# Optimization experiments

Measured on AMD Instinct MI355X. Metric: run time of the kernel, lower is better.

## Reference

```python
import jax, jax.numpy as jnp
import numpy as np

B, D, H, W, K = 32, 32, 256, 256, 512
N_TAGS = 30


def setup_inputs() -> dict:
    key = jax.random.key(0)
    k1, k2, k3 = jax.random.split(key, 3)
    ebd_batch = jax.random.normal(k1, (B, D, H, W), dtype=jnp.float32)
    # integer pixel coords (row, col) already in-range -> mask in original is all-true
    kpts = jax.random.randint(k2, (B, K, 2), 0, H).astype(jnp.int64)
    tags = jax.random.randint(k3, (B, K), 0, N_TAGS).astype(jnp.int64)
    return {"ebd_batch": ebd_batch, "kpts": kpts, "tags": tags}


def _per_image(ebd, kp, tg):
    # ebd: [D,H,W], kp: [K,2] int, tg: [K] int
    pred = ebd[:, kp[:, 0], kp[:, 1]]            # [D,K] gathered embeddings
    d = pred.shape[0]
    true_sim = (tg[:, None] == tg[None, :]).astype(pred.dtype)   # [K,K]
    # expo[k,l] = mean_d (pred[d,k]-pred[d,l])^2, via gram expansion (no DxKxK tensor)
    sq = jnp.mean(pred * pred, axis=0)           # [K]
    gram = jnp.einsum('dk,dl->kl', pred, pred) / d
    expo = sq[:, None] + sq[None, :] - 2.0 * gram
    pred_sim = 2.0 / (1.0 + jnp.exp(expo))
    return jnp.mean((true_sim - pred_sim) ** 2)


def reference(ebd_batch, kpts, tags):
    losses = jax.vmap(_per_image)(ebd_batch, kpts, tags)  # [B]
    return jnp.mean(losses)
```

## Files before the change

kernel.cpp:

```cpp
#include <hip/hip_runtime.h>

#define BB 32
#define DD 32
#define HH 256
#define WW 256
#define KK 512

typedef __attribute__((ext_vector_type(8))) short bf16x8;
typedef __attribute__((ext_vector_type(4))) float f32x4;

#define LO_OFF  (1u << 20)
#define SSQ_OFF (2u << 20)

__global__ __launch_bounds__(256) void tagloss_gather(
    const float* __restrict__ ebd, const int* __restrict__ kpts,
    char* __restrict__ ws, float* __restrict__ out) {
  int gid = blockIdx.x * 256 + threadIdx.x;
  if (gid == 0) out[0] = 0.f;
  int col = gid >> 5;
  int d   = gid & 31;
  int b   = col >> 9;

  int y = kpts[col * 2 + 0];
  int x = kpts[col * 2 + 1];
  float v = ebd[((size_t)(b * DD + d)) * (HH * WW) + (size_t)y * WW + x];

  unsigned u  = __float_as_uint(v);
  unsigned rn = u + 0x7FFFu + ((u >> 16) & 1u);
  float hif = __uint_as_float(rn & 0xFFFF0000u);
  float lof = v - hif;
  unsigned ul = __float_as_uint(lof);
  unsigned rl = ul + 0x7FFFu + ((ul >> 16) & 1u);

  ((ushort*)ws)[col * DD + d]            = (ushort)(rn >> 16);
  ((ushort*)(ws + LO_OFF))[col * DD + d] = (ushort)(rl >> 16);

  float s = v * v;
#pragma unroll
  for (int m = 16; m > 0; m >>= 1) s += __shfl_xor(s, m);
  if (d == 0) ((float*)(ws + SSQ_OFF))[col] = s;
}

__global__ __launch_bounds__(256, 2) void tagloss_pairs(
    const char* __restrict__ ws, const int* __restrict__ tags,
    float* __restrict__ out) {
  __shared__ __align__(16) char P[65536];
  __shared__ float ssqL[KK];
  __shared__ int   tagL[KK];
  __shared__ float red[4];

  const int tid = threadIdx.x;
  const int b = blockIdx.y;
  const int p = blockIdx.x;

#pragma unroll
  for (int i = 0; i < 16; ++i) {
    int j = tid + i * 256;
    int plane = j >> 11;
    int col = (j >> 2) & 511;
    int dc = j & 3;
    const float4* src = (const float4*)(ws + (size_t)plane * LO_OFF +
                                        (size_t)b * 32768 + col * 64 + dc * 16);
    *(float4*)(P + plane * 32768 + col * 64 + ((dc ^ ((col >> 1) & 3)) * 16)) = *src;
  }
  ssqL[tid]       = ((const float*)(ws + SSQ_OFF))[b * KK + tid];
  ssqL[tid + 256] = ((const float*)(ws + SSQ_OFF))[b * KK + tid + 256];
  tagL[tid]       = tags[b * KK + tid];
  tagL[tid + 256] = tags[b * KK + tid + 256];
  __syncthreads();

  const int w = tid >> 6, lane = tid & 63;
  const int lx = lane & 15, dchunk = lane >> 4;

  const int i0 = p, i1 = 31 - p;
  const int lim = 32 - i0;

  const int colA0 = i0 * 16 + lx;
  const int colA1 = i1 * 16 + lx;
  const int swzA0 = ((dchunk ^ ((colA0 >> 1) & 3)) * 16);
  const int swzA1 = ((dchunk ^ ((colA1 >> 1) & 3)) * 16);
  bf16x8 a0hi = *(const bf16x8*)(P + colA0 * 64 + swzA0);
  bf16x8 a0lo = *(const bf16x8*)(P + 32768 + colA0 * 64 + swzA0);
  bf16x8 a1hi = *(const bf16x8*)(P + colA1 * 64 + swzA1);
  bf16x8 a1lo = *(const bf16x8*)(P + 32768 + colA1 * 64 + swzA1);

  const int krow0 = i0 * 16 + dchunk * 4;
  const int krow1 = i1 * 16 + dchunk * 4;
  float ssqk0[4], ssqk1[4];
  int   tagk0[4], tagk1[4];
#pragma unroll
  for (int r = 0; r < 4; ++r) {
    ssqk0[r] = ssqL[krow0 + r]; tagk0[r] = tagL[krow0 + r];
    ssqk1[r] = ssqL[krow1 + r]; tagk1[r] = tagL[krow1 + r];
  }

  float loss = 0.f;

#define JOB(AHI, ALO, SSQK, TAGK, KT, JT)                                      \
  {                                                                            \
    const int colB = (JT) * 16 + lx;                                           \
    const int swzB = ((dchunk ^ ((colB >> 1) & 3)) * 16);                      \
    bf16x8 bhi = *(const bf16x8*)(P + colB * 64 + swzB);                       \
    bf16x8 blo = *(const bf16x8*)(P + 32768 + colB * 64 + swzB);               \
    f32x4 acc = {0.f, 0.f, 0.f, 0.f};                                          \
    acc = __builtin_amdgcn_mfma_f32_16x16x32_bf16(ALO, bhi, acc, 0, 0, 0);     \
    acc = __builtin_amdgcn_mfma_f32_16x16x32_bf16(AHI, blo, acc, 0, 0, 0);     \
    acc = __builtin_amdgcn_mfma_f32_16x16x32_bf16(AHI, bhi, acc, 0, 0, 0);     \
    float ssql = ssqL[colB];                                                   \
    int   tagl = tagL[colB];                                                   \
    float jobLoss = 0.f;                                                       \
    _Pragma("unroll")                                                          \
    for (int r = 0; r < 4; ++r) {                                              \
      float expo = (SSQK[r] + ssql - 2.f * acc[r]) * 0.03125f;                 \
      float ps = 2.f * __builtin_amdgcn_rcpf(1.f + __expf(expo));              \
      float t = (TAGK[r] == tagl) ? 1.f : 0.f;                                 \
      float df = t - ps;                                                       \
      jobLoss = fmaf(df, df, jobLoss);                                         \
    }                                                                          \
    float wtf = ((KT) == (JT)) ? 1.f : 2.f;                                    \
    loss = fmaf(jobLoss, wtf, loss);                                           \
  }

  for (int t = w; t < lim; t += 4) JOB(a0hi, a0lo, ssqk0, tagk0, i0, i0 + t);
  {
    int m0 = (lim > w) ? ((lim - w + 3) >> 2) : 0;
    for (int t = w + 4 * m0; t < 33; t += 4)
      JOB(a1hi, a1lo, ssqk1, tagk1, i1, i1 + (t - lim));
  }
#undef JOB

#pragma unroll
  for (int off = 32; off > 0; off >>= 1) loss += __shfl_down(loss, off);
  if (lane == 0) red[w] = loss;
  __syncthreads();
  if (tid == 0)
    atomicAdd(out, (red[0] + red[1] + red[2] + red[3]) * (1.f / 8388608.f));
}

extern "C" void kernel_launch(void* const* d_in, const int* in_sizes, int n_in,
                              void* d_out, int out_size, void* d_ws, size_t ws_size,
                              hipStream_t stream) {
  const float* ebd  = (const float*)d_in[0];
  const int*   kpts = (const int*)d_in[1];
  const int*   tags = (const int*)d_in[2];
  float* out = (float*)d_out;

  tagloss_gather<<<(BB * KK * DD) / 256, 256, 0, stream>>>(ebd, kpts, (char*)d_ws, out);
  tagloss_pairs<<<dim3(16, BB), 256, 0, stream>>>((const char*)d_ws, tags, out);
}
```

Baseline: 27.35 us.

## Pack hi/lo bf16 into one word and compute sum-of-squares in pairs kernel

The gather kernel now writes one packed 32-bit word per element holding the hi and lo bf16 halves, and it reorders the thread mapping so consecutive threads handle consecutive keypoints. The per-column sum-of-squares reduction and its separate store move out of the gather kernel. The pairs kernel now unpacks the words with byte-perm into the two swizzled LDS planes and rebuilds the squared norms from hi+lo. This cuts shuffle work and stores in the gather kernel, but the norms now come from the bf16 split rather than exact fp32, and the LDS fill step gains extra work and an extra barrier.

```diff
diff --git a/kernel.cpp b/kernel.cpp
--- a/kernel.cpp
+++ b/kernel.cpp
@@ -9,21 +9,18 @@
 typedef __attribute__((ext_vector_type(8))) short bf16x8;
 typedef __attribute__((ext_vector_type(4))) float f32x4;
 
-#define LO_OFF  (1u << 20)
-#define SSQ_OFF (2u << 20)
 
 __global__ __launch_bounds__(256) void tagloss_gather(
     const float* __restrict__ ebd, const int* __restrict__ kpts,
-    char* __restrict__ ws, float* __restrict__ out) {
+    unsigned* __restrict__ wsU, float* __restrict__ out) {
   int gid = blockIdx.x * 256 + threadIdx.x;
   if (gid == 0) out[0] = 0.f;
-  int col = gid >> 5;
-  int d   = gid & 31;
+  int col = gid & 16383;
+  int d   = gid >> 14;
   int b   = col >> 9;
 
-  int y = kpts[col * 2 + 0];
-  int x = kpts[col * 2 + 1];
-  float v = ebd[((size_t)(b * DD + d)) * (HH * WW) + (size_t)y * WW + x];
+  int2 kp = ((const int2*)kpts)[col];
+  float v = ebd[((size_t)(b * DD + d)) * (HH * WW) + (size_t)kp.x * WW + kp.y];
 
   unsigned u  = __float_as_uint(v);
   unsigned rn = u + 0x7FFFu + ((u >> 16) & 1u);
@@ -32,19 +29,14 @@
   unsigned ul = __float_as_uint(lof);
   unsigned rl = ul + 0x7FFFu + ((ul >> 16) & 1u);
 
-  ((ushort*)ws)[col * DD + d]            = (ushort)(rn >> 16);
-  ((ushort*)(ws + LO_OFF))[col * DD + d] = (ushort)(rl >> 16);
-
-  float s = v * v;
-#pragma unroll
-  for (int m = 16; m > 0; m >>= 1) s += __shfl_xor(s, m);
-  if (d == 0) ((float*)(ws + SSQ_OFF))[col] = s;
+  wsU[col * DD + d] = (rn >> 16) | (rl & 0xFFFF0000u);
 }
 
 __global__ __launch_bounds__(256, 2) void tagloss_pairs(
     const char* __restrict__ ws, const int* __restrict__ tags,
     float* __restrict__ out) {
   __shared__ __align__(16) char P[65536];
+  __shared__ float ssqP[2048];
   __shared__ float ssqL[KK];
   __shared__ int   tagL[KK];
   __shared__ float red[4];
@@ -53,20 +45,48 @@
   const int b = blockIdx.y;
   const int p = blockIdx.x;
 
+  const char* wsb = ws + (size_t)b * 65536;
 #pragma unroll
-  for (int i = 0; i < 16; ++i) {
-    int j = tid + i * 256;
-    int plane = j >> 11;
-    int col = (j >> 2) & 511;
-    int dc = j & 3;
-    const float4* src = (const float4*)(ws + (size_t)plane * LO_OFF +
-                                        (size_t)b * 32768 + col * 64 + dc * 16);
-    *(float4*)(P + plane * 32768 + col * 64 + ((dc ^ ((col >> 1) & 3)) * 16)) = *src;
+  for (int i = 0; i < 8; ++i) {
+    int slot = tid + i * 256;
+    int col = slot >> 2, pc = slot & 3;
+    const uint4* g = (const uint4*)(wsb + col * 128 + pc * 32);
+    uint4 ga = g[0], gb = g[1];
+
+    unsigned h0 = __builtin_amdgcn_perm(ga.y, ga.x, 0x05040100u);
+    unsigned h1 = __builtin_amdgcn_perm(ga.w, ga.z, 0x05040100u);
+    unsigned h2 = __builtin_amdgcn_perm(gb.y, gb.x, 0x05040100u);
+    unsigned h3 = __builtin_amdgcn_perm(gb.w, gb.z, 0x05040100u);
+    unsigned l0 = __builtin_amdgcn_perm(ga.y, ga.x, 0x07060302u);
+    unsigned l1 = __builtin_amdgcn_perm(ga.w, ga.z, 0x07060302u);
+    unsigned l2 = __builtin_amdgcn_perm(gb.y, gb.x, 0x07060302u);
+    unsigned l3 = __builtin_amdgcn_perm(gb.w, gb.z, 0x07060302u);
+
+    int phys = pc ^ ((col >> 1) & 3);
+    *(uint4*)(P + col * 64 + phys * 16)         = make_uint4(h0, h1, h2, h3);
+    *(uint4*)(P + 32768 + col * 64 + phys * 16) = make_uint4(l0, l1, l2, l3);
+
+    float s = 0.f;
+    unsigned wv[8] = {ga.x, ga.y, ga.z, ga.w, gb.x, gb.y, gb.z, gb.w};
+#pragma unroll
+    for (int q = 0; q < 8; ++q) {
+      float hf = __uint_as_float(wv[q] << 16);
+      float lf = __uint_as_float(wv[q] & 0xFFFF0000u);
+      float vf = hf + lf;
+      s = fmaf(vf, vf, s);
+    }
+    ssqP[slot] = s;
   }
-  ssqL[tid]       = ((const float*)(ws + SSQ_OFF))[b * KK + tid];
-  ssqL[tid + 256] = ((const float*)(ws + SSQ_OFF))[b * KK + tid + 256];
   tagL[tid]       = tags[b * KK + tid];
   tagL[tid + 256] = tags[b * KK + tid + 256];
+  __syncthreads();
+
+#pragma unroll
+  for (int i = 0; i < 2; ++i) {
+    int c = tid + i * 256;
+    f32x4 q = *(const f32x4*)&ssqP[c * 4];
+    ssqL[c] = (q[0] + q[1]) + (q[2] + q[3]);
+  }
   __syncthreads();
 
   const int w = tid >> 6, lane = tid & 63;
@@ -145,6 +165,7 @@
   const int*   tags = (const int*)d_in[2];
   float* out = (float*)d_out;
 
-  tagloss_gather<<<(BB * KK * DD) / 256, 256, 0, stream>>>(ebd, kpts, (char*)d_ws, out);
+  tagloss_gather<<<(BB * KK * DD) / 256, 256, 0, stream>>>(
+      ebd, kpts, (unsigned*)d_ws, out);
   tagloss_pairs<<<dim3(16, BB), 256, 0, stream>>>((const char*)d_ws, tags, out);
 }
```

New measurement: 28.53 us. +4.3%, slower.
